# Kernel optimization log

Hardware: AMD Instinct MI355X
Metric: run time of the kernel (lower is better)

The kernel has to match this reference:

```python
import jax, jax.numpy as jnp
import numpy as np
from jax import lax

B, D, DEPTH, H, P, NP, IMG, PS = 16, 384, 6, 6, 2000, 4, 224, 16
N = (IMG // PS) ** 2  # 196 patches
T = N + 1             # +cls token
TEMP = 100.0
NEG = -100000.0


def layernorm(x, s, b, eps=1e-6):
    m = jnp.mean(x, -1, keepdims=True)
    v = jnp.var(x, -1, keepdims=True)
    return (x - m) * lax.rsqrt(v + eps) * s + b


def setup_inputs() -> dict:
    key = jax.random.key(0)
    ks = jax.random.split(key, 16)
    s = 0.02
    inp = {
        "x": jax.random.normal(ks[0], (B, 3, IMG, IMG), jnp.float32),
        "patch_w": jax.random.normal(ks[1], (D, 3, PS, PS), jnp.float32) * s,
        "patch_b": jnp.zeros((D,), jnp.float32),
        "cls_token": jax.random.normal(ks[2], (1, 1, D), jnp.float32) * s,
        "pos_embed": jax.random.normal(ks[3], (1, T, D), jnp.float32) * s,
        "ln1_s": jnp.ones((DEPTH, D), jnp.float32),
        "ln1_b": jnp.zeros((DEPTH, D), jnp.float32),
        "qkv_w": jax.random.normal(ks[4], (DEPTH, D, 3 * D), jnp.float32) * s,
        "qkv_b": jnp.zeros((DEPTH, 3 * D), jnp.float32),
        "proj_w": jax.random.normal(ks[5], (DEPTH, D, D), jnp.float32) * s,
        "proj_b": jnp.zeros((DEPTH, D), jnp.float32),
        "ln2_s": jnp.ones((DEPTH, D), jnp.float32),
        "ln2_b": jnp.zeros((DEPTH, D), jnp.float32),
        "fc1_w": jax.random.normal(ks[6], (DEPTH, D, 4 * D), jnp.float32) * s,
        "fc1_b": jnp.zeros((DEPTH, 4 * D), jnp.float32),
        "fc2_w": jax.random.normal(ks[7], (DEPTH, 4 * D, D), jnp.float32) * s,
        "fc2_b": jnp.zeros((DEPTH, D), jnp.float32),
        "norm_s": jnp.ones((D,), jnp.float32),
        "norm_b": jnp.zeros((D,), jnp.float32),
        "proto": jax.random.normal(ks[8], (P, D, NP), jnp.float32),
        "patch_select": jnp.full((1, P, NP), 0.1, jnp.float32),
    }
    return inp


def vit_features(x, patch_w, patch_b, cls_token, pos_embed, blk, norm_s, norm_b):
    # patch embed: non-overlapping 16x16 conv, NCHW/OIHW
    f = lax.conv_general_dilated(x, patch_w, (PS, PS), "VALID",
                                 dimension_numbers=("NCHW", "OIHW", "NCHW"))
    f = f + patch_b[None, :, None, None]              # (B, D, 14, 14)
    tok = f.reshape(B, D, N).transpose(0, 2, 1)        # (B, N, D)
    tok = jnp.concatenate([jnp.broadcast_to(cls_token, (B, 1, D)), tok], axis=1)
    tok = tok + pos_embed

    hd = D // H
    scale = hd ** -0.5

    def block(t, p):
        l1s, l1b, qw, qb, pw, pb, l2s, l2b, f1w, f1b, f2w, f2b = p
        h = layernorm(t, l1s, l1b)
        qkv = h @ qw + qb                              # (B, T, 3D)
        q, k, v = jnp.split(qkv, 3, axis=-1)
        q = q.reshape(B, T, H, hd).transpose(0, 2, 1, 3)
        k = k.reshape(B, T, H, hd).transpose(0, 2, 1, 3)
        v = v.reshape(B, T, H, hd).transpose(0, 2, 1, 3)
        att = jax.nn.softmax(jnp.einsum("bhqd,bhkd->bhqk", q, k) * scale, axis=-1)
        o = jnp.einsum("bhqk,bhkd->bhqd", att, v).transpose(0, 2, 1, 3).reshape(B, T, D)
        t = t + (o @ pw + pb)
        h = layernorm(t, l2s, l2b)
        t = t + (jax.nn.gelu(h @ f1w + f1b, approximate=False) @ f2w + f2b)
        return t, None

    tok, _ = lax.scan(block, tok, blk)
    tok = layernorm(tok, norm_s, norm_b)
    cls = tok[:, 0]                                    # (B, D)
    x_focal = tok[:, 1:] - cls[:, None, :]             # (B, N, D)
    feat = x_focal.transpose(0, 2, 1)                  # (B, D, N) == (B,D,14,14) flat
    return feat, cls


def reference(x, patch_w, patch_b, cls_token, pos_embed, ln1_s, ln1_b, qkv_w,
              qkv_b, proj_w, proj_b, ln2_s, ln2_b, fc1_w, fc1_b, fc2_w, fc2_b,
              norm_s, norm_b, proto, patch_select):
    blk = (ln1_s, ln1_b, qkv_w, qkv_b, proj_w, proj_b, ln2_s, ln2_b,
           fc1_w, fc1_b, fc2_w, fc2_b)
    feat, cls = vit_features(x, patch_w, patch_b, cls_token, pos_embed, blk,
                             norm_s, norm_b)
    # L2-normalize over channel dim (torch F.normalize, eps=1e-12)
    fn = feat / jnp.maximum(jnp.linalg.norm(feat, axis=1, keepdims=True), 1e-12)
    pn = proto / jnp.maximum(jnp.linalg.norm(proto, axis=1, keepdims=True), 1e-12)
    # cosine sims for every (prototype, patch, subpatch): (B, P, N, NP)
    dist = jnp.einsum("bdn,pdk->bpnk", fn, pn).reshape(B, P, N * NP)

    slots = jax.nn.sigmoid(patch_select * TEMP)        # (1, P, NP)
    factor = slots.sum(-1, keepdims=True) + 1e-10

    mask = jnp.ones((B, P, N * NP), dist.dtype)
    col = jnp.arange(N * NP)
    vals = []
    for _ in range(NP):  # greedy non-overlapping subpatch matching
        dm = dist + (1.0 - mask) * NEG
        ids = jnp.argmax(dm, axis=-1)                  # (B, P)
        vals.append(jnp.take_along_axis(dm, ids[..., None], axis=-1)[..., 0])
        mask = jnp.where(col[None, None, :] == ids[..., None], 0.0, mask)
    values = jnp.stack(vals, axis=-1)                  # (B, P, NP)
    proto_scores = (values * (slots * NP / factor)).sum(-1)  # (B, P)
    return cls, proto_scores
```

## Files before the change

kernel.cpp:

```cpp
#include <hip/hip_runtime.h>
#include <hip/hip_bf16.h>
#include <math.h>


#define MROWS 3152

typedef short bf16x8 __attribute__((ext_vector_type(8)));
typedef float f32x4 __attribute__((ext_vector_type(4)));
typedef unsigned short u16;

__device__ __forceinline__ void async_copy16(void* lds, const void* g) {
    __builtin_amdgcn_global_load_lds((const __attribute__((address_space(1))) unsigned int*)g,
                                     (__attribute__((address_space(3))) unsigned int*)lds,
                                     16, 0, 0);
}

__device__ __forceinline__ u16 f2b(float x) {
    __hip_bfloat16 h = __float2bfloat16(x);
    return *(u16*)&h;
}

__global__ void k_cvt(const float* __restrict__ in, __hip_bfloat16* __restrict__ o, int n) {
    int i = blockIdx.x * 256 + threadIdx.x;
    if (i < n) o[i] = __float2bfloat16(in[i]);
}

__global__ __launch_bounds__(256) void k_wt(const float* __restrict__ W, __hip_bfloat16* __restrict__ Wt,
                                            int K, int N) {
    __shared__ float t[32][33];
    const float* src = W + (size_t)blockIdx.z * K * N;
    __hip_bfloat16* dst = Wt + (size_t)blockIdx.z * K * N;
    int n0 = blockIdx.x * 32, k0 = blockIdx.y * 32;
    int tx = threadIdx.x & 31, ty = threadIdx.x >> 5;
    #pragma unroll
    for (int i = 0; i < 4; ++i) t[ty + i * 8][tx] = src[(size_t)(k0 + ty + i * 8) * N + n0 + tx];
    __syncthreads();
    #pragma unroll
    for (int i = 0; i < 4; ++i)
        dst[(size_t)(n0 + ty + i * 8) * K + k0 + tx] = __float2bfloat16(t[tx][ty + i * 8]);
}

__global__ void k_im2col(const float* __restrict__ x, __hip_bfloat16* __restrict__ Acol) {
    int idx = blockIdx.x * 256 + threadIdx.x;
    int k = idx % 768;
    int m = idx / 768;
    int b = m / 196, n = m % 196;
    int c = k >> 8, rem = k & 255, i = rem >> 4, j = rem & 15;
    int py = n / 14, px = n % 14;
    Acol[idx] = __float2bfloat16(x[((b * 3 + c) * 224 + py * 16 + i) * 224 + px * 16 + j]);
}

template<int RES, int GELU, int BF16OUT>
__global__ __launch_bounds__(256) void k_mfma_gemm(
    const u16* __restrict__ A, const u16* __restrict__ Bt,
    const float* __restrict__ bias, const float* __restrict__ res,
    float* __restrict__ Cf, __hip_bfloat16* __restrict__ Cb,
    int M, int N, int K)
{
    __shared__ u16 As[2][128 * 64];
    __shared__ u16 Bs[2][128 * 64];
    const int tid = threadIdx.x;
    const int wid = tid >> 6, lane = tid & 63;
    const int m0 = blockIdx.y * 128, n0 = blockIdx.x * 128;
    const int srow = tid >> 3;
    const int selem = (tid & 7) << 3;
    const int wm = (wid >> 1) * 64, wn = (wid & 1) * 64;

    f32x4 acc[4][4] = {};

    auto stage = [&](int buf, int kb) {
        #pragma unroll
        for (int g = 0; g < 4; ++g) {
            int r = g * 32 + srow;
            int sw = selem ^ ((r & 7) << 3);
            int gr = m0 + r; if (gr > M - 1) gr = M - 1;
            async_copy16(&As[buf][r * 64 + selem], A + (size_t)gr * K + kb + sw);
            async_copy16(&Bs[buf][r * 64 + selem], Bt + (size_t)(n0 + r) * K + kb + sw);
        }
    };

    const int nk = K >> 6;
    stage(0, 0);
    __syncthreads();
    for (int t = 0; t < nk; ++t) {
        const int cur = t & 1;
        if (t + 1 < nk) stage(cur ^ 1, (t + 1) << 6);
        #pragma unroll
        for (int ks = 0; ks < 64; ks += 32) {
            const int kk = ks + ((lane >> 4) << 3);
            bf16x8 af[4], bfr[4];
            #pragma unroll
            for (int i = 0; i < 4; ++i) {
                int r = wm + i * 16 + (lane & 15);
                af[i] = *(const bf16x8*)&As[cur][r * 64 + (kk ^ ((r & 7) << 3))];
            }
            #pragma unroll
            for (int j = 0; j < 4; ++j) {
                int r = wn + j * 16 + (lane & 15);
                bfr[j] = *(const bf16x8*)&Bs[cur][r * 64 + (kk ^ ((r & 7) << 3))];
            }
            #pragma unroll
            for (int i = 0; i < 4; ++i)
                #pragma unroll
                for (int j = 0; j < 4; ++j)
                    acc[i][j] = __builtin_amdgcn_mfma_f32_16x16x32_bf16(af[i], bfr[j], acc[i][j], 0, 0, 0);
        }
        __syncthreads();
    }
    const int cl = lane & 15, rg = (lane >> 4) << 2;
    #pragma unroll
    for (int i = 0; i < 4; ++i) {
        #pragma unroll
        for (int j = 0; j < 4; ++j) {
            const int col = n0 + wn + j * 16 + cl;
            const float bv = bias[col];
            #pragma unroll
            for (int r = 0; r < 4; ++r) {
                const int row = m0 + wm + i * 16 + rg + r;
                if (row >= M) continue;
                float v = acc[i][j][r] + bv;
                if (RES) v += res[(size_t)row * N + col];
                if (GELU) v = 0.5f * v * (1.0f + erff(v * 0.70710678118f));
                if (BF16OUT) Cb[(size_t)row * N + col] = __float2bfloat16(v);
                else         Cf[(size_t)row * N + col] = v;
            }
        }
    }
}

template<int RES, int GELU, int BF16OUT>
__global__ __launch_bounds__(256) void k_mfma_gemm64(
    const u16* __restrict__ A, const u16* __restrict__ Bt,
    const float* __restrict__ bias, const float* __restrict__ res,
    float* __restrict__ Cf, __hip_bfloat16* __restrict__ Cb,
    int M, int N, int K)
{
    __shared__ u16 As[2][128 * 64];
    __shared__ u16 Bs[2][64 * 64];
    const int tid = threadIdx.x;
    const int wid = tid >> 6, lane = tid & 63;
    const int m0 = blockIdx.y * 128, n0 = blockIdx.x * 64;
    const int srow = tid >> 3;
    const int selem = (tid & 7) << 3;
    const int wm = wid * 32;

    f32x4 acc[2][4] = {};

    auto stage = [&](int buf, int kb) {
        #pragma unroll
        for (int g = 0; g < 4; ++g) {
            int r = g * 32 + srow;
            int sw = selem ^ ((r & 7) << 3);
            int gr = m0 + r; if (gr > M - 1) gr = M - 1;
            async_copy16(&As[buf][r * 64 + selem], A + (size_t)gr * K + kb + sw);
        }
        #pragma unroll
        for (int g = 0; g < 2; ++g) {
            int r = g * 32 + srow;
            int sw = selem ^ ((r & 7) << 3);
            async_copy16(&Bs[buf][r * 64 + selem], Bt + (size_t)(n0 + r) * K + kb + sw);
        }
    };

    const int nk = K >> 6;
    stage(0, 0);
    __syncthreads();
    for (int t = 0; t < nk; ++t) {
        const int cur = t & 1;
        if (t + 1 < nk) stage(cur ^ 1, (t + 1) << 6);
        #pragma unroll
        for (int ks = 0; ks < 64; ks += 32) {
            const int kk = ks + ((lane >> 4) << 3);
            bf16x8 af[2], bfr[4];
            #pragma unroll
            for (int i = 0; i < 2; ++i) {
                int r = wm + i * 16 + (lane & 15);
                af[i] = *(const bf16x8*)&As[cur][r * 64 + (kk ^ ((r & 7) << 3))];
            }
            #pragma unroll
            for (int j = 0; j < 4; ++j) {
                int r = j * 16 + (lane & 15);
                bfr[j] = *(const bf16x8*)&Bs[cur][r * 64 + (kk ^ ((r & 7) << 3))];
            }
            #pragma unroll
            for (int i = 0; i < 2; ++i)
                #pragma unroll
                for (int j = 0; j < 4; ++j)
                    acc[i][j] = __builtin_amdgcn_mfma_f32_16x16x32_bf16(af[i], bfr[j], acc[i][j], 0, 0, 0);
        }
        __syncthreads();
    }
    const int cl = lane & 15, rg = (lane >> 4) << 2;
    #pragma unroll
    for (int i = 0; i < 2; ++i) {
        #pragma unroll
        for (int j = 0; j < 4; ++j) {
            const int col = n0 + j * 16 + cl;
            const float bv = bias[col];
            #pragma unroll
            for (int r = 0; r < 4; ++r) {
                const int row = m0 + wm + i * 16 + rg + r;
                if (row >= M) continue;
                float v = acc[i][j][r] + bv;
                if (RES) v += res[(size_t)row * N + col];
                if (GELU) v = 0.5f * v * (1.0f + erff(v * 0.70710678118f));
                if (BF16OUT) Cb[(size_t)row * N + col] = __float2bfloat16(v);
                else         Cf[(size_t)row * N + col] = v;
            }
        }
    }
}

__global__ void k_assemble(const float* __restrict__ ptmp, const float* __restrict__ cls_tok,
                           const float* __restrict__ pos, float* __restrict__ tok) {
    int idx = blockIdx.x * 256 + threadIdx.x;
    int d = idx % 384;
    int t = (idx / 384) % 197;
    int b = idx / (384 * 197);
    float v = (t == 0) ? cls_tok[d] : ptmp[((size_t)b * 196 + t - 1) * 384 + d];
    tok[idx] = v + pos[t * 384 + d];
}

template<typename OT>
__global__ __launch_bounds__(256) void k_ln(const float* __restrict__ X, const float* __restrict__ s,
                                            const float* __restrict__ bb, OT* __restrict__ Y, int rows) {
    int wid = threadIdx.x >> 6, lane = threadIdx.x & 63;
    int row = blockIdx.x * 4 + wid;
    if (row >= rows) return;
    const float* x = X + (size_t)row * 384;
    float v[6], sum = 0.f, sq = 0.f;
    #pragma unroll
    for (int i = 0; i < 6; ++i) { float t = x[lane + 64 * i]; v[i] = t; sum += t; sq += t * t; }
    #pragma unroll
    for (int m = 32; m > 0; m >>= 1) { sum += __shfl_xor(sum, m); sq += __shfl_xor(sq, m); }
    float mean = sum * (1.f / 384.f);
    float var  = sq * (1.f / 384.f) - mean * mean;
    float rstd = rsqrtf(var + 1e-6f);
    OT* y = Y + (size_t)row * 384;
    #pragma unroll
    for (int i = 0; i < 6; ++i) {
        int d = lane + 64 * i;
        float o = (v[i] - mean) * rstd * s[d] + bb[d];
        y[d] = (OT)o;
    }
}

__global__ __launch_bounds__(256) void k_attn_mfma(const u16* __restrict__ qkv, u16* __restrict__ o) {
    __shared__ u16 Ks[208 * 64];
    __shared__ u16 VT[64 * 256];
    __shared__ u16 Pl[4][16 * 256];
    const int bh = blockIdx.x;
    const int b = bh / 6, hh = bh % 6;
    const u16* base = qkv + (size_t)b * 197 * 1152 + hh * 64;
    const int tid = threadIdx.x, wid = tid >> 6, lane = tid & 63;

    for (int i = tid; i < 64 * 59; i += 256) {
        int d = i / 59, k = 197 + i % 59;
        VT[d * 256 + (k ^ ((d & 7) << 3))] = 0;
    }
    for (int i = tid; i < 64 * 48; i += 256) {
        int q = i / 48, k = 208 + i % 48;
        Pl[q >> 4][(q & 15) * 256 + (k ^ ((q & 7) << 3))] = 0;
    }
    for (int i = tid; i < 197 * 8; i += 256) {
        int r = i >> 3, cc = (i & 7) << 3;
        uint4 v = *(const uint4*)(base + (size_t)r * 1152 + 384 + cc);
        *(uint4*)&Ks[r * 64 + (cc ^ ((r & 7) << 3))] = v;
    }
    for (int i = tid; i < 197 * 8; i += 256) {
        int r = i >> 3, d0 = (i & 7) << 3;
        uint4 v = *(const uint4*)(base + (size_t)r * 1152 + 768 + d0);
        const u16* pv = (const u16*)&v;
        #pragma unroll
        for (int j = 0; j < 8; ++j) {
            int d = d0 + j;
            VT[d * 256 + (r ^ ((d & 7) << 3))] = pv[j];
        }
    }
    __syncthreads();

    const int g = lane >> 4, c = lane & 15;
    const int t0 = blockIdx.y * 7;
    const int nt = blockIdx.y ? 6 : 7;
    for (int t = wid; t < nt; t += 4) {
        const int qt = t0 + t;
        const int q0 = qt * 16;
        int qrow = q0 + c; if (qrow > 196) qrow = 196;
        bf16x8 aq[2];
        aq[0] = *(const bf16x8*)(base + (size_t)qrow * 1152 + g * 8);
        aq[1] = *(const bf16x8*)(base + (size_t)qrow * 1152 + 32 + g * 8);

        f32x4 acc[13] = {};
        #pragma unroll
        for (int j = 0; j < 13; ++j) {
            int kr = j * 16 + c;
            bf16x8 b0 = *(const bf16x8*)&Ks[kr * 64 + ((g * 8) ^ ((kr & 7) << 3))];
            bf16x8 b1 = *(const bf16x8*)&Ks[kr * 64 + ((32 + g * 8) ^ ((kr & 7) << 3))];
            acc[j] = __builtin_amdgcn_mfma_f32_16x16x32_bf16(aq[0], b0, acc[j], 0, 0, 0);
            acc[j] = __builtin_amdgcn_mfma_f32_16x16x32_bf16(aq[1], b1, acc[j], 0, 0, 0);
        }

        float sc[13][4];
        float mr[4] = {-1e30f, -1e30f, -1e30f, -1e30f};
        #pragma unroll
        for (int j = 0; j < 13; ++j) {
            bool valid = (j * 16 + c) < 197;
            #pragma unroll
            for (int r = 0; r < 4; ++r) {
                float v = valid ? acc[j][r] * 0.125f : -1e30f;
                sc[j][r] = v;
                mr[r] = fmaxf(mr[r], v);
            }
        }
        #pragma unroll
        for (int r = 0; r < 4; ++r) {
            #pragma unroll
            for (int msk = 1; msk <= 8; msk <<= 1) mr[r] = fmaxf(mr[r], __shfl_xor(mr[r], msk));
        }
        float lr[4] = {0.f, 0.f, 0.f, 0.f};
        #pragma unroll
        for (int j = 0; j < 13; ++j)
            #pragma unroll
            for (int r = 0; r < 4; ++r) { float e = __expf(sc[j][r] - mr[r]); sc[j][r] = e; lr[r] += e; }
        #pragma unroll
        for (int r = 0; r < 4; ++r) {
            #pragma unroll
            for (int msk = 1; msk <= 8; msk <<= 1) lr[r] += __shfl_xor(lr[r], msk);
            lr[r] = 1.f / lr[r];
        }
        #pragma unroll
        for (int j = 0; j < 13; ++j) {
            int col = j * 16 + c;
            #pragma unroll
            for (int r = 0; r < 4; ++r) {
                int q = g * 4 + r;
                Pl[wid][q * 256 + (col ^ ((q & 7) << 3))] = f2b(sc[j][r] * lr[r]);
            }
        }
        asm volatile("s_waitcnt lgkmcnt(0)" ::: "memory");

        f32x4 av[4] = {};
        #pragma unroll
        for (int ks = 0; ks < 7; ++ks) {
            int kk = ks * 32 + g * 8;
            bf16x8 ap = *(const bf16x8*)&Pl[wid][c * 256 + (kk ^ ((c & 7) << 3))];
            #pragma unroll
            for (int jd = 0; jd < 4; ++jd) {
                int dr = jd * 16 + c;
                bf16x8 bv = *(const bf16x8*)&VT[dr * 256 + (kk ^ ((dr & 7) << 3))];
                av[jd] = __builtin_amdgcn_mfma_f32_16x16x32_bf16(ap, bv, av[jd], 0, 0, 0);
            }
        }
        #pragma unroll
        for (int jd = 0; jd < 4; ++jd) {
            #pragma unroll
            for (int r = 0; r < 4; ++r) {
                int q = q0 + g * 4 + r;
                if (q < 197)
                    o[((size_t)b * 197 + q) * 384 + hh * 64 + jd * 16 + c] = f2b(av[jd][r]);
            }
        }
    }
}

__global__ __launch_bounds__(256) void k_fn(const float* __restrict__ tokn, __hip_bfloat16* __restrict__ fn,
                                            float* __restrict__ out) {
    int wid = threadIdx.x >> 6, lane = threadIdx.x & 63;
    int row = blockIdx.x * 4 + wid;
    int b = row / 196, n = row % 196;
    const float* xr = tokn + ((size_t)b * 197 + 1 + n) * 384;
    const float* cr = tokn + (size_t)b * 197 * 384;
    float v[6], ss = 0.f;
    #pragma unroll
    for (int i = 0; i < 6; ++i) {
        int d = lane + 64 * i;
        float t = xr[d] - cr[d];
        v[i] = t; ss += t * t;
    }
    #pragma unroll
    for (int m = 32; m > 0; m >>= 1) ss += __shfl_xor(ss, m);
    float inv = 1.f / fmaxf(sqrtf(ss), 1e-12f);
    #pragma unroll
    for (int i = 0; i < 6; ++i) fn[(size_t)row * 384 + lane + 64 * i] = __float2bfloat16(v[i] * inv);
    int idx = blockIdx.x * 256 + threadIdx.x;
    if (idx < 6144) out[idx] = tokn[(size_t)(idx / 384) * 197 * 384 + idx % 384];
}

__global__ __launch_bounds__(256) void k_pn(const float* __restrict__ proto, __hip_bfloat16* __restrict__ pn) {
    int p = blockIdx.x;
    int k = threadIdx.x >> 6, lane = threadIdx.x & 63;
    float v[6], ss = 0.f;
    #pragma unroll
    for (int i = 0; i < 6; ++i) {
        int d = lane + 64 * i;
        float t = proto[((size_t)p * 384 + d) * 4 + k];
        v[i] = t; ss += t * t;
    }
    #pragma unroll
    for (int m = 32; m > 0; m >>= 1) ss += __shfl_xor(ss, m);
    float inv = 1.f / fmaxf(sqrtf(ss), 1e-12f);
    #pragma unroll
    for (int i = 0; i < 6; ++i) pn[((size_t)p * 4 + k) * 384 + lane + 64 * i] = __float2bfloat16(v[i] * inv);
}

__device__ __forceinline__ void top4_insert(float v, float& t0, float& t1, float& t2, float& t3) {
    if (v > t3) {
        t3 = v;
        if (t3 > t2) { float t = t2; t2 = t3; t3 = t; }
        if (t2 > t1) { float t = t1; t1 = t2; t2 = t; }
        if (t1 > t0) { float t = t0; t0 = t1; t1 = t; }
    }
}

__global__ __launch_bounds__(256) void k_dist_mfma(
    const __hip_bfloat16* __restrict__ fnb, const __hip_bfloat16* __restrict__ pnb,
    const float* __restrict__ psel, float* __restrict__ out)
{
    __shared__ u16 Ap[128 * 64];
    __shared__ u16 Bf[208 * 64];
    const u16* fn = (const u16*)fnb;
    const u16* pn = (const u16*)pnb;
    const int b = blockIdx.x;
    const int pb = blockIdx.y;
    const int tid = threadIdx.x, wid = tid >> 6, lane = tid & 63;
    const int srow = tid >> 3;
    const int selem = (tid & 7) << 3;

    f32x4 acc[2][13] = {};

    for (int kt = 0; kt < 384; kt += 64) {
        __syncthreads();
        #pragma unroll
        for (int g = 0; g < 4; ++g) {
            int r = g * 32 + srow;
            int gr = pb * 128 + r; if (gr > 7999) gr = 7999;
            async_copy16(&Ap[r * 64 + selem],
                         pn + (size_t)gr * 384 + kt + (selem ^ ((r & 7) << 3)));
        }
        #pragma unroll
        for (int g = 0; g < 7; ++g) {
            int r = g * 32 + srow;
            if (r < 208) {
                int fr = r > 195 ? 195 : r;
                async_copy16(&Bf[r * 64 + selem],
                             fn + ((size_t)b * 196 + fr) * 384 + kt + (selem ^ ((r & 7) << 3)));
            }
        }
        __syncthreads();
        #pragma unroll
        for (int ks = 0; ks < 64; ks += 32) {
            const int kk = ks + ((lane >> 4) << 3);
            bf16x8 af[2];
            #pragma unroll
            for (int i = 0; i < 2; ++i) {
                int r = wid * 32 + i * 16 + (lane & 15);
                af[i] = *(const bf16x8*)&Ap[r * 64 + (kk ^ ((r & 7) << 3))];
            }
            #pragma unroll
            for (int j = 0; j < 13; ++j) {
                int r = j * 16 + (lane & 15);
                bf16x8 bj = *(const bf16x8*)&Bf[r * 64 + (kk ^ ((r & 7) << 3))];
                acc[0][j] = __builtin_amdgcn_mfma_f32_16x16x32_bf16(af[0], bj, acc[0][j], 0, 0, 0);
                acc[1][j] = __builtin_amdgcn_mfma_f32_16x16x32_bf16(af[1], bj, acc[1][j], 0, 0, 0);
            }
        }
    }
    const int cl = lane & 15;
    #pragma unroll
    for (int mi = 0; mi < 2; ++mi) {
        float t0 = -1e30f, t1 = -1e30f, t2 = -1e30f, t3 = -1e30f;
        #pragma unroll
        for (int j = 0; j < 13; ++j) {
            if (j * 16 + cl >= 196) continue;
            #pragma unroll
            for (int r = 0; r < 4; ++r) top4_insert(acc[mi][j][r], t0, t1, t2, t3);
        }
        #pragma unroll
        for (int m = 1; m <= 8; m <<= 1) {
            float u0 = __shfl_xor(t0, m), u1 = __shfl_xor(t1, m);
            float u2 = __shfl_xor(t2, m), u3 = __shfl_xor(t3, m);
            top4_insert(u0, t0, t1, t2, t3);
            top4_insert(u1, t0, t1, t2, t3);
            top4_insert(u2, t0, t1, t2, t3);
            top4_insert(u3, t0, t1, t2, t3);
        }
        if (cl == 0) {
            int proto = pb * 32 + wid * 8 + mi * 4 + (lane >> 4);
            if (proto < 2000) {
                float sl[4], fac = 1e-10f;
                #pragma unroll
                for (int i = 0; i < 4; ++i) {
                    sl[i] = 1.f / (1.f + expf(-psel[proto * 4 + i] * 100.f));
                    fac += sl[i];
                }
                float score = (t0 * sl[0] + t1 * sl[1] + t2 * sl[2] + t3 * sl[3]) * 4.f / fac;
                out[6144 + (size_t)b * 2000 + proto] = score;
            }
        }
    }
}

extern "C" void kernel_launch(void* const* d_in, const int* in_sizes, int n_in,
                              void* d_out, int out_size, void* d_ws, size_t ws_size,
                              hipStream_t stream) {
    const float* x       = (const float*)d_in[0];
    const float* patch_w = (const float*)d_in[1];
    const float* patch_b = (const float*)d_in[2];
    const float* cls_tok = (const float*)d_in[3];
    const float* pos     = (const float*)d_in[4];
    const float* ln1_s   = (const float*)d_in[5];
    const float* ln1_b   = (const float*)d_in[6];
    const float* qkv_w   = (const float*)d_in[7];
    const float* qkv_b   = (const float*)d_in[8];
    const float* proj_w  = (const float*)d_in[9];
    const float* proj_b  = (const float*)d_in[10];
    const float* ln2_s   = (const float*)d_in[11];
    const float* ln2_b   = (const float*)d_in[12];
    const float* fc1_w   = (const float*)d_in[13];
    const float* fc1_b   = (const float*)d_in[14];
    const float* fc2_w   = (const float*)d_in[15];
    const float* fc2_b   = (const float*)d_in[16];
    const float* norm_s  = (const float*)d_in[17];
    const float* norm_b  = (const float*)d_in[18];
    const float* proto   = (const float*)d_in[19];
    const float* psel    = (const float*)d_in[20];
    float* out = (float*)d_out;
    char* w = (char*)d_ws;

    __hip_bfloat16* wPb  = (__hip_bfloat16*)(w);
    __hip_bfloat16* wQ   = (__hip_bfloat16*)(w + 589824);
    __hip_bfloat16* wPr  = (__hip_bfloat16*)(w + 5898240);
    __hip_bfloat16* wF1  = (__hip_bfloat16*)(w + 7667712);
    __hip_bfloat16* wF2  = (__hip_bfloat16*)(w + 14745600);
    __hip_bfloat16* Acol = (__hip_bfloat16*)(w + 21823488);
    float*          ptmp = (float*)         (w + 26640384);
    float*          tok  = (float*)         (w + 31457280);
    __hip_bfloat16* hbf  = (__hip_bfloat16*)(w + 36298752);
    __hip_bfloat16* qkvb = (__hip_bfloat16*)(w + 38719488);
    __hip_bfloat16* aob  = (__hip_bfloat16*)(w + 53243904);
    __hip_bfloat16* hbig = (__hip_bfloat16*)(w + 55664640);
    float*          hf   = (float*)         (w + 65347584);
    __hip_bfloat16* fnb  = (__hip_bfloat16*)(w + 70189056);
    __hip_bfloat16* pnb  = (__hip_bfloat16*)(w + 72597504);

    k_cvt<<<1152, 256, 0, stream>>>(patch_w, wPb, 294912);
    k_wt<<<dim3(36, 12, 6), 256, 0, stream>>>(qkv_w, wQ, 384, 1152);
    k_wt<<<dim3(12, 12, 6), 256, 0, stream>>>(proj_w, wPr, 384, 384);
    k_wt<<<dim3(48, 12, 6), 256, 0, stream>>>(fc1_w, wF1, 384, 1536);
    k_wt<<<dim3(12, 48, 6), 256, 0, stream>>>(fc2_w, wF2, 1536, 384);

    k_im2col<<<9408, 256, 0, stream>>>(x, Acol);
    k_mfma_gemm64<0,0,0><<<dim3(6, 25), 256, 0, stream>>>(
        (const u16*)Acol, (const u16*)wPb, patch_b, nullptr, ptmp, nullptr, 3136, 384, 768);
    k_assemble<<<4728, 256, 0, stream>>>(ptmp, cls_tok, pos, tok);

    for (int l = 0; l < 6; ++l) {
        k_ln<__hip_bfloat16><<<788, 256, 0, stream>>>(tok, ln1_s + l * 384, ln1_b + l * 384, hbf, MROWS);
        k_mfma_gemm<0,0,1><<<dim3(9, 25), 256, 0, stream>>>(
            (const u16*)hbf, (const u16*)(wQ + (size_t)l * 1152 * 384), qkv_b + l * 1152,
            nullptr, nullptr, qkvb, MROWS, 1152, 384);
        k_attn_mfma<<<dim3(96, 2), 256, 0, stream>>>((const u16*)qkvb, (u16*)aob);
        k_mfma_gemm64<1,0,0><<<dim3(6, 25), 256, 0, stream>>>(
            (const u16*)aob, (const u16*)(wPr + (size_t)l * 384 * 384), proj_b + l * 384,
            tok, tok, nullptr, MROWS, 384, 384);
        k_ln<__hip_bfloat16><<<788, 256, 0, stream>>>(tok, ln2_s + l * 384, ln2_b + l * 384, hbf, MROWS);
        k_mfma_gemm<0,1,1><<<dim3(12, 25), 256, 0, stream>>>(
            (const u16*)hbf, (const u16*)(wF1 + (size_t)l * 1536 * 384), fc1_b + l * 1536,
            nullptr, nullptr, hbig, MROWS, 1536, 384);
        k_mfma_gemm64<1,0,0><<<dim3(6, 25), 256, 0, stream>>>(
            (const u16*)hbig, (const u16*)(wF2 + (size_t)l * 384 * 1536), fc2_b + l * 384,
            tok, tok, nullptr, MROWS, 384, 1536);
    }

    k_ln<float><<<788, 256, 0, stream>>>(tok, norm_s, norm_b, hf, MROWS);
    k_fn<<<784, 256, 0, stream>>>(hf, fnb, out);
    k_pn<<<2000, 256, 0, stream>>>(proto, pnb);
    k_dist_mfma<<<dim3(16, 63), 256, 0, stream>>>(fnb, pnb, psel, out);
}
```

Baseline: 685.6 us.

## Fuse layernorm into GEMM prologues and merge prep kernels into one launch

LayerNorm is folded into the QKV and FC1 GEMMs. Each block computes row statistics, then normalizes fp32 tokens into bf16 LDS tiles while staging B asynchronously, so the separate LN kernels and the hbf round-trip go away. All weight conversion, transposes, im2col, prototype normalization and cls-token init are merged into a single k_prep launch. Patch-embed now writes tokens plus pos embedding directly, and final LN is fused with feature normalization. This cuts launches and memory traffic, but the GEMM blocks take on redundant per-tile LN statistic work and register pressure.

```diff
diff --git a/kernel.cpp b/kernel.cpp
--- a/kernel.cpp
+++ b/kernel.cpp
@@ -20,18 +20,14 @@
     return *(u16*)&h;
 }
 
-__global__ void k_cvt(const float* __restrict__ in, __hip_bfloat16* __restrict__ o, int n) {
-    int i = blockIdx.x * 256 + threadIdx.x;
-    if (i < n) o[i] = __float2bfloat16(in[i]);
-}
-
-__global__ __launch_bounds__(256) void k_wt(const float* __restrict__ W, __hip_bfloat16* __restrict__ Wt,
-                                            int K, int N) {
-    __shared__ float t[32][33];
-    const float* src = W + (size_t)blockIdx.z * K * N;
-    __hip_bfloat16* dst = Wt + (size_t)blockIdx.z * K * N;
-    int n0 = blockIdx.x * 32, k0 = blockIdx.y * 32;
-    int tx = threadIdx.x & 31, ty = threadIdx.x >> 5;
+__device__ __forceinline__ void wt_tile(const float* __restrict__ W, __hip_bfloat16* __restrict__ Wt,
+                                        int K, int N, int id, int ntx, int perlayer,
+                                        float (*t)[33], int tid) {
+    int z = id / perlayer, rem = id % perlayer;
+    int n0 = (rem % ntx) * 32, k0 = (rem / ntx) * 32;
+    const float* src = W + (size_t)z * K * N;
+    __hip_bfloat16* dst = Wt + (size_t)z * K * N;
+    int tx = tid & 31, ty = tid >> 5;
     #pragma unroll
     for (int i = 0; i < 4; ++i) t[ty + i * 8][tx] = src[(size_t)(k0 + ty + i * 8) * N + n0 + tx];
     __syncthreads();
@@ -40,33 +36,82 @@
         dst[(size_t)(n0 + ty + i * 8) * K + k0 + tx] = __float2bfloat16(t[tx][ty + i * 8]);
 }
 
-__global__ void k_im2col(const float* __restrict__ x, __hip_bfloat16* __restrict__ Acol) {
-    int idx = blockIdx.x * 256 + threadIdx.x;
-    int k = idx % 768;
-    int m = idx / 768;
-    int b = m / 196, n = m % 196;
-    int c = k >> 8, rem = k & 255, i = rem >> 4, j = rem & 15;
-    int py = n / 14, px = n % 14;
-    Acol[idx] = __float2bfloat16(x[((b * 3 + c) * 224 + py * 16 + i) * 224 + px * 16 + j]);
-}
-
-template<int RES, int GELU, int BF16OUT>
-__global__ __launch_bounds__(256) void k_mfma_gemm(
+__global__ __launch_bounds__(256) void k_prep(
+    const float* __restrict__ patch_w, __hip_bfloat16* __restrict__ wPb,
+    const float* __restrict__ cls_tok, const float* __restrict__ pos, float* __restrict__ tok,
+    const float* __restrict__ qkv_w, __hip_bfloat16* __restrict__ wQ,
+    const float* __restrict__ proj_w, __hip_bfloat16* __restrict__ wPr,
+    const float* __restrict__ fc1_w, __hip_bfloat16* __restrict__ wF1,
+    const float* __restrict__ fc2_w, __hip_bfloat16* __restrict__ wF2,
+    const float* __restrict__ x, __hip_bfloat16* __restrict__ Acol,
+    const float* __restrict__ proto, __hip_bfloat16* __restrict__ pn)
+{
+    __shared__ float t[32][33];
+    int bid = blockIdx.x;
+    const int tid = threadIdx.x;
+    if (bid < 1152) {
+        int i = bid * 256 + tid;
+        wPb[i] = __float2bfloat16(patch_w[i]);
+        if (i < 6144) {
+            int b = i / 384, d = i % 384;
+            tok[(size_t)b * 197 * 384 + d] = cls_tok[d] + pos[d];
+        }
+        return;
+    }
+    bid -= 1152;
+    if (bid < 2592) { wt_tile(qkv_w, wQ, 384, 1152, bid, 36, 432, t, tid); return; }
+    bid -= 2592;
+    if (bid < 864)  { wt_tile(proj_w, wPr, 384, 384, bid, 12, 144, t, tid); return; }
+    bid -= 864;
+    if (bid < 3456) { wt_tile(fc1_w, wF1, 384, 1536, bid, 48, 576, t, tid); return; }
+    bid -= 3456;
+    if (bid < 3456) { wt_tile(fc2_w, wF2, 1536, 384, bid, 12, 576, t, tid); return; }
+    bid -= 3456;
+    if (bid < 9408) {
+        int idx = bid * 256 + tid;
+        int k = idx % 768, m = idx / 768;
+        int b = m / 196, n = m % 196;
+        int c = k >> 8, rem = k & 255, i = rem >> 4, j = rem & 15;
+        int py = n / 14, px = n % 14;
+        Acol[idx] = __float2bfloat16(x[((b * 3 + c) * 224 + py * 16 + i) * 224 + px * 16 + j]);
+        return;
+    }
+    bid -= 9408;
+    {
+        int p = bid;
+        int k = tid >> 6, lane = tid & 63;
+        float v[6], ss = 0.f;
+        #pragma unroll
+        for (int i = 0; i < 6; ++i) {
+            int d = lane + 64 * i;
+            float tv = proto[((size_t)p * 384 + d) * 4 + k];
+            v[i] = tv; ss += tv * tv;
+        }
+        #pragma unroll
+        for (int m = 32; m > 0; m >>= 1) ss += __shfl_xor(ss, m);
+        float inv = 1.f / fmaxf(sqrtf(ss), 1e-12f);
+        #pragma unroll
+        for (int i = 0; i < 6; ++i)
+            pn[((size_t)p * 4 + k) * 384 + lane + 64 * i] = __float2bfloat16(v[i] * inv);
+    }
+}
+
+__global__ __launch_bounds__(256) void k_patch_tok(
     const u16* __restrict__ A, const u16* __restrict__ Bt,
-    const float* __restrict__ bias, const float* __restrict__ res,
-    float* __restrict__ Cf, __hip_bfloat16* __restrict__ Cb,
-    int M, int N, int K)
+    const float* __restrict__ bias, const float* __restrict__ pos,
+    float* __restrict__ tok)
 {
+    const int M = 3136, K = 768;
     __shared__ u16 As[2][128 * 64];
-    __shared__ u16 Bs[2][128 * 64];
+    __shared__ u16 Bs[2][64 * 64];
     const int tid = threadIdx.x;
     const int wid = tid >> 6, lane = tid & 63;
-    const int m0 = blockIdx.y * 128, n0 = blockIdx.x * 128;
+    const int m0 = blockIdx.y * 128, n0 = blockIdx.x * 64;
     const int srow = tid >> 3;
     const int selem = (tid & 7) << 3;
-    const int wm = (wid >> 1) * 64, wn = (wid & 1) * 64;
-
-    f32x4 acc[4][4] = {};
+    const int wm = wid * 32;
+
+    f32x4 acc[2][4] = {};
 
     auto stage = [&](int buf, int kb) {
         #pragma unroll
@@ -75,6 +120,11 @@
             int sw = selem ^ ((r & 7) << 3);
             int gr = m0 + r; if (gr > M - 1) gr = M - 1;
             async_copy16(&As[buf][r * 64 + selem], A + (size_t)gr * K + kb + sw);
+        }
+        #pragma unroll
+        for (int g = 0; g < 2; ++g) {
+            int r = g * 32 + srow;
+            int sw = selem ^ ((r & 7) << 3);
             async_copy16(&Bs[buf][r * 64 + selem], Bt + (size_t)(n0 + r) * K + kb + sw);
         }
     };
@@ -88,6 +138,126 @@
         #pragma unroll
         for (int ks = 0; ks < 64; ks += 32) {
             const int kk = ks + ((lane >> 4) << 3);
+            bf16x8 af[2], bfr[4];
+            #pragma unroll
+            for (int i = 0; i < 2; ++i) {
+                int r = wm + i * 16 + (lane & 15);
+                af[i] = *(const bf16x8*)&As[cur][r * 64 + (kk ^ ((r & 7) << 3))];
+            }
+            #pragma unroll
+            for (int j = 0; j < 4; ++j) {
+                int r = j * 16 + (lane & 15);
+                bfr[j] = *(const bf16x8*)&Bs[cur][r * 64 + (kk ^ ((r & 7) << 3))];
+            }
+            #pragma unroll
+            for (int i = 0; i < 2; ++i)
+                #pragma unroll
+                for (int j = 0; j < 4; ++j)
+                    acc[i][j] = __builtin_amdgcn_mfma_f32_16x16x32_bf16(af[i], bfr[j], acc[i][j], 0, 0, 0);
+        }
+        __syncthreads();
+    }
+    const int cl = lane & 15, rg = (lane >> 4) << 2;
+    #pragma unroll
+    for (int i = 0; i < 2; ++i) {
+        #pragma unroll
+        for (int j = 0; j < 4; ++j) {
+            const int col = n0 + j * 16 + cl;
+            const float bv = bias[col];
+            #pragma unroll
+            for (int r = 0; r < 4; ++r) {
+                const int row = m0 + wm + i * 16 + rg + r;
+                if (row >= M) continue;
+                int b = row / 196, n = row % 196;
+                float v = acc[i][j][r] + bv + pos[(size_t)(1 + n) * 384 + col];
+                tok[((size_t)b * 197 + 1 + n) * 384 + col] = v;
+            }
+        }
+    }
+}
+
+template<int GELU>
+__global__ __launch_bounds__(256) void k_gemm_ln(
+    const float* __restrict__ tokf, const float* __restrict__ lns, const float* __restrict__ lnb,
+    const u16* __restrict__ Bt, const float* __restrict__ bias,
+    u16* __restrict__ Cb, int N)
+{
+    __shared__ u16 As[2][128 * 64];
+    __shared__ u16 Bs[2][128 * 64];
+    __shared__ float st[128][2];
+    __shared__ __align__(16) float sg[384];
+    __shared__ __align__(16) float bg[384];
+    const int tid = threadIdx.x, wid = tid >> 6, lane = tid & 63;
+    const int m0 = blockIdx.y * 128, n0 = blockIdx.x * 128;
+    const int srow = tid >> 3, selem = (tid & 7) << 3;
+    const int wm = (wid >> 1) * 64, wn = (wid & 1) * 64;
+
+    for (int i = tid; i < 384; i += 256) { sg[i] = lns[i]; bg[i] = lnb[i]; }
+    for (int i = 0; i < 32; ++i) {
+        int rl = wid + 4 * i;
+        int gr = m0 + rl; if (gr > MROWS - 1) gr = MROWS - 1;
+        const float* xr = tokf + (size_t)gr * 384;
+        float sum = 0.f, sq = 0.f;
+        #pragma unroll
+        for (int j = 0; j < 6; ++j) { float tv = xr[lane + 64 * j]; sum += tv; sq += tv * tv; }
+        #pragma unroll
+        for (int m = 32; m > 0; m >>= 1) { sum += __shfl_xor(sum, m); sq += __shfl_xor(sq, m); }
+        if (lane == 0) {
+            float mean = sum * (1.f / 384.f);
+            st[rl][0] = mean;
+            st[rl][1] = rsqrtf(sq * (1.f / 384.f) - mean * mean + 1e-6f);
+        }
+    }
+    __syncthreads();
+
+    const int r_ = tid >> 1, half = tid & 1, c0 = half * 32;
+    const float mean = st[r_][0], rstd = st[r_][1];
+    int gr_ = m0 + r_; if (gr_ > MROWS - 1) gr_ = MROWS - 1;
+    const float* arow = tokf + (size_t)gr_ * 384;
+
+    float4 areg[8];
+    auto loadA = [&](int kb) {
+        #pragma unroll
+        for (int c = 0; c < 8; ++c) areg[c] = *(const float4*)(arow + kb + c0 + c * 4);
+    };
+    auto writeA = [&](int buf, int kb) {
+        #pragma unroll
+        for (int c = 0; c < 4; ++c) {
+            const int colb = kb + c0 + c * 8;
+            float4 s0 = *(const float4*)&sg[colb], s1 = *(const float4*)&sg[colb + 4];
+            float4 b0 = *(const float4*)&bg[colb], b1 = *(const float4*)&bg[colb + 4];
+            float va[8] = {areg[2*c].x, areg[2*c].y, areg[2*c].z, areg[2*c].w,
+                           areg[2*c+1].x, areg[2*c+1].y, areg[2*c+1].z, areg[2*c+1].w};
+            float ss[8] = {s0.x, s0.y, s0.z, s0.w, s1.x, s1.y, s1.z, s1.w};
+            float bb[8] = {b0.x, b0.y, b0.z, b0.w, b1.x, b1.y, b1.z, b1.w};
+            bf16x8 pk;
+            #pragma unroll
+            for (int e = 0; e < 8; ++e)
+                pk[e] = (short)f2b((va[e] - mean) * rstd * ss[e] + bb[e]);
+            int chunk = (half * 4 + c) ^ (r_ & 7);
+            *(bf16x8*)&As[buf][r_ * 64 + chunk * 8] = pk;
+        }
+    };
+    auto stageB = [&](int buf, int kb) {
+        #pragma unroll
+        for (int g = 0; g < 4; ++g) {
+            int r = g * 32 + srow;
+            int sw = selem ^ ((r & 7) << 3);
+            async_copy16(&Bs[buf][r * 64 + selem], Bt + (size_t)(n0 + r) * 384 + kb + sw);
+        }
+    };
+
+    f32x4 acc[4][4] = {};
+    loadA(0);
+    stageB(0, 0);
+    writeA(0, 0);
+    __syncthreads();
+    for (int t = 0; t < 6; ++t) {
+        const int cur = t & 1;
+        if (t < 5) { loadA((t + 1) << 6); stageB(cur ^ 1, (t + 1) << 6); }
+        #pragma unroll
+        for (int ks = 0; ks < 64; ks += 32) {
+            const int kk = ks + ((lane >> 4) << 3);
             bf16x8 af[4], bfr[4];
             #pragma unroll
             for (int i = 0; i < 4; ++i) {
@@ -105,6 +275,7 @@
                 for (int j = 0; j < 4; ++j)
                     acc[i][j] = __builtin_amdgcn_mfma_f32_16x16x32_bf16(af[i], bfr[j], acc[i][j], 0, 0, 0);
         }
+        if (t < 5) writeA(cur ^ 1, (t + 1) << 6);
         __syncthreads();
     }
     const int cl = lane & 15, rg = (lane >> 4) << 2;
@@ -117,12 +288,10 @@
             #pragma unroll
             for (int r = 0; r < 4; ++r) {
                 const int row = m0 + wm + i * 16 + rg + r;
-                if (row >= M) continue;
+                if (row >= MROWS) continue;
                 float v = acc[i][j][r] + bv;
-                if (RES) v += res[(size_t)row * N + col];
                 if (GELU) v = 0.5f * v * (1.0f + erff(v * 0.70710678118f));
-                if (BF16OUT) Cb[(size_t)row * N + col] = __float2bfloat16(v);
-                else         Cf[(size_t)row * N + col] = v;
+                Cb[(size_t)row * N + col] = f2b(v);
             }
         }
     }
@@ -211,40 +380,6 @@
     }
 }
 
-__global__ void k_assemble(const float* __restrict__ ptmp, const float* __restrict__ cls_tok,
-                           const float* __restrict__ pos, float* __restrict__ tok) {
-    int idx = blockIdx.x * 256 + threadIdx.x;
-    int d = idx % 384;
-    int t = (idx / 384) % 197;
-    int b = idx / (384 * 197);
-    float v = (t == 0) ? cls_tok[d] : ptmp[((size_t)b * 196 + t - 1) * 384 + d];
-    tok[idx] = v + pos[t * 384 + d];
-}
-
-template<typename OT>
-__global__ __launch_bounds__(256) void k_ln(const float* __restrict__ X, const float* __restrict__ s,
-                                            const float* __restrict__ bb, OT* __restrict__ Y, int rows) {
-    int wid = threadIdx.x >> 6, lane = threadIdx.x & 63;
-    int row = blockIdx.x * 4 + wid;
-    if (row >= rows) return;
-    const float* x = X + (size_t)row * 384;
-    float v[6], sum = 0.f, sq = 0.f;
-    #pragma unroll
-    for (int i = 0; i < 6; ++i) { float t = x[lane + 64 * i]; v[i] = t; sum += t; sq += t * t; }
-    #pragma unroll
-    for (int m = 32; m > 0; m >>= 1) { sum += __shfl_xor(sum, m); sq += __shfl_xor(sq, m); }
-    float mean = sum * (1.f / 384.f);
-    float var  = sq * (1.f / 384.f) - mean * mean;
-    float rstd = rsqrtf(var + 1e-6f);
-    OT* y = Y + (size_t)row * 384;
-    #pragma unroll
-    for (int i = 0; i < 6; ++i) {
-        int d = lane + 64 * i;
-        float o = (v[i] - mean) * rstd * s[d] + bb[d];
-        y[d] = (OT)o;
-    }
-}
-
 __global__ __launch_bounds__(256) void k_attn_mfma(const u16* __restrict__ qkv, u16* __restrict__ o) {
     __shared__ u16 Ks[208 * 64];
     __shared__ u16 VT[64 * 256];
@@ -283,8 +418,7 @@
     const int t0 = blockIdx.y * 7;
     const int nt = blockIdx.y ? 6 : 7;
     for (int t = wid; t < nt; t += 4) {
-        const int qt = t0 + t;
-        const int q0 = qt * 16;
+        const int q0 = (t0 + t) * 16;
         int qrow = q0 + c; if (qrow > 196) qrow = 196;
         bf16x8 aq[2];
         aq[0] = *(const bf16x8*)(base + (size_t)qrow * 1152 + g * 8);
@@ -363,44 +497,47 @@
     }
 }
 
-__global__ __launch_bounds__(256) void k_fn(const float* __restrict__ tokn, __hip_bfloat16* __restrict__ fn,
-                                            float* __restrict__ out) {
+__device__ __forceinline__ void lnvals(const float* __restrict__ x, const float* __restrict__ s,
+                                       const float* __restrict__ bb, int lane, float* v) {
+    float sum = 0.f, sq = 0.f;
+    #pragma unroll
+    for (int i = 0; i < 6; ++i) { float t = x[lane + 64 * i]; v[i] = t; sum += t; sq += t * t; }
+    #pragma unroll
+    for (int m = 32; m > 0; m >>= 1) { sum += __shfl_xor(sum, m); sq += __shfl_xor(sq, m); }
+    float mean = sum * (1.f / 384.f);
+    float var  = sq * (1.f / 384.f) - mean * mean;
+    float rstd = rsqrtf(var + 1e-6f);
+    #pragma unroll
+    for (int i = 0; i < 6; ++i) {
+        int d = lane + 64 * i;
+        v[i] = (v[i] - mean) * rstd * s[d] + bb[d];
+    }
+}
+
+__global__ __launch_bounds__(256) void k_fnln(const float* __restrict__ tok, const float* __restrict__ s,
+                                              const float* __restrict__ bb, u16* __restrict__ fnb,
+                                              float* __restrict__ out) {
     int wid = threadIdx.x >> 6, lane = threadIdx.x & 63;
     int row = blockIdx.x * 4 + wid;
-    int b = row / 196, n = row % 196;
-    const float* xr = tokn + ((size_t)b * 197 + 1 + n) * 384;
-    const float* cr = tokn + (size_t)b * 197 * 384;
-    float v[6], ss = 0.f;
-    #pragma unroll
-    for (int i = 0; i < 6; ++i) {
-        int d = lane + 64 * i;
-        float t = xr[d] - cr[d];
-        v[i] = t; ss += t * t;
-    }
-    #pragma unroll
-    for (int m = 32; m > 0; m >>= 1) ss += __shfl_xor(ss, m);
-    float inv = 1.f / fmaxf(sqrtf(ss), 1e-12f);
-    #pragma unroll
-    for (int i = 0; i < 6; ++i) fn[(size_t)row * 384 + lane + 64 * i] = __float2bfloat16(v[i] * inv);
-    int idx = blockIdx.x * 256 + threadIdx.x;
-    if (idx < 6144) out[idx] = tokn[(size_t)(idx / 384) * 197 * 384 + idx % 384];
-}
-
-__global__ __launch_bounds__(256) void k_pn(const float* __restrict__ proto, __hip_bfloat16* __restrict__ pn) {
-    int p = blockIdx.x;
-    int k = threadIdx.x >> 6, lane = threadIdx.x & 63;
-    float v[6], ss = 0.f;
-    #pragma unroll
-    for (int i = 0; i < 6; ++i) {
-        int d = lane + 64 * i;
-        float t = proto[((size_t)p * 384 + d) * 4 + k];
-        v[i] = t; ss += t * t;
-    }
-    #pragma unroll
-    for (int m = 32; m > 0; m >>= 1) ss += __shfl_xor(ss, m);
-    float inv = 1.f / fmaxf(sqrtf(ss), 1e-12f);
-    #pragma unroll
-    for (int i = 0; i < 6; ++i) pn[((size_t)p * 4 + k) * 384 + lane + 64 * i] = __float2bfloat16(v[i] * inv);
+    int b = row / 197, t = row % 197;
+    float v1[6];
+    lnvals(tok + (size_t)row * 384, s, bb, lane, v1);
+    if (t == 0) {
+        #pragma unroll
+        for (int i = 0; i < 6; ++i) out[(size_t)b * 384 + lane + 64 * i] = v1[i];
+    } else {
+        float v0[6];
+        lnvals(tok + (size_t)b * 197 * 384, s, bb, lane, v0);
+        float d[6], ss = 0.f;
+        #pragma unroll
+        for (int i = 0; i < 6; ++i) { d[i] = v1[i] - v0[i]; ss += d[i] * d[i]; }
+        #pragma unroll
+        for (int m = 32; m > 0; m >>= 1) ss += __shfl_xor(ss, m);
+        float inv = 1.f / fmaxf(sqrtf(ss), 1e-12f);
+        #pragma unroll
+        for (int i = 0; i < 6; ++i)
+            fnb[((size_t)b * 196 + t - 1) * 384 + lane + 64 * i] = f2b(d[i] * inv);
+    }
 }
 
 __device__ __forceinline__ void top4_insert(float v, float& t0, float& t1, float& t2, float& t3) {
@@ -528,52 +665,42 @@
     char* w = (char*)d_ws;
 
     __hip_bfloat16* wPb  = (__hip_bfloat16*)(w);
-    __hip_bfloat16* wQ   = (__hip_bfloat16*)(w + 589824);
-    __hip_bfloat16* wPr  = (__hip_bfloat16*)(w + 5898240);
-    __hip_bfloat16* wF1  = (__hip_bfloat16*)(w + 7667712);
-    __hip_bfloat16* wF2  = (__hip_bfloat16*)(w + 14745600);
+    u16*            wQ   = (u16*)(w + 589824);
+    u16*            wPr  = (u16*)(w + 5898240);
+    u16*            wF1  = (u16*)(w + 7667712);
+    u16*            wF2  = (u16*)(w + 14745600);
     __hip_bfloat16* Acol = (__hip_bfloat16*)(w + 21823488);
-    float*          ptmp = (float*)         (w + 26640384);
     float*          tok  = (float*)         (w + 31457280);
-    __hip_bfloat16* hbf  = (__hip_bfloat16*)(w + 36298752);
-    __hip_bfloat16* qkvb = (__hip_bfloat16*)(w + 38719488);
-    __hip_bfloat16* aob  = (__hip_bfloat16*)(w + 53243904);
-    __hip_bfloat16* hbig = (__hip_bfloat16*)(w + 55664640);
-    float*          hf   = (float*)         (w + 65347584);
-    __hip_bfloat16* fnb  = (__hip_bfloat16*)(w + 70189056);
+    u16*            qkvb = (u16*)(w + 38719488);
+    u16*            aob  = (u16*)(w + 53243904);
+    u16*            hbig = (u16*)(w + 55664640);
+    u16*            fnb  = (u16*)(w + 70189056);
     __hip_bfloat16* pnb  = (__hip_bfloat16*)(w + 72597504);
 
-    k_cvt<<<1152, 256, 0, stream>>>(patch_w, wPb, 294912);
-    k_wt<<<dim3(36, 12, 6), 256, 0, stream>>>(qkv_w, wQ, 384, 1152);
-    k_wt<<<dim3(12, 12, 6), 256, 0, stream>>>(proj_w, wPr, 384, 384);
-    k_wt<<<dim3(48, 12, 6), 256, 0, stream>>>(fc1_w, wF1, 384, 1536);
-    k_wt<<<dim3(12, 48, 6), 256, 0, stream>>>(fc2_w, wF2, 1536, 384);
-
-    k_im2col<<<9408, 256, 0, stream>>>(x, Acol);
-    k_mfma_gemm64<0,0,0><<<dim3(6, 25), 256, 0, stream>>>(
-        (const u16*)Acol, (const u16*)wPb, patch_b, nullptr, ptmp, nullptr, 3136, 384, 768);
-    k_assemble<<<4728, 256, 0, stream>>>(ptmp, cls_tok, pos, tok);
+    k_prep<<<22928, 256, 0, stream>>>(patch_w, wPb, cls_tok, pos, tok,
+                                      qkv_w, (__hip_bfloat16*)wQ,
+                                      proj_w, (__hip_bfloat16*)wPr,
+                                      fc1_w, (__hip_bfloat16*)wF1,
+                                      fc2_w, (__hip_bfloat16*)wF2,
+                                      x, Acol, proto, pnb);
+    k_patch_tok<<<dim3(6, 25), 256, 0, stream>>>((const u16*)Acol, (const u16*)wPb, patch_b, pos, tok);
 
     for (int l = 0; l < 6; ++l) {
-        k_ln<__hip_bfloat16><<<788, 256, 0, stream>>>(tok, ln1_s + l * 384, ln1_b + l * 384, hbf, MROWS);
-        k_mfma_gemm<0,0,1><<<dim3(9, 25), 256, 0, stream>>>(
-            (const u16*)hbf, (const u16*)(wQ + (size_t)l * 1152 * 384), qkv_b + l * 1152,
-            nullptr, nullptr, qkvb, MROWS, 1152, 384);
-        k_attn_mfma<<<dim3(96, 2), 256, 0, stream>>>((const u16*)qkvb, (u16*)aob);
+        k_gemm_ln<0><<<dim3(9, 25), 256, 0, stream>>>(
+            tok, ln1_s + l * 384, ln1_b + l * 384,
+            wQ + (size_t)l * 1152 * 384, qkv_b + l * 1152, qkvb, 1152);
+        k_attn_mfma<<<dim3(96, 2), 256, 0, stream>>>(qkvb, aob);
         k_mfma_gemm64<1,0,0><<<dim3(6, 25), 256, 0, stream>>>(
-            (const u16*)aob, (const u16*)(wPr + (size_t)l * 384 * 384), proj_b + l * 384,
+            aob, wPr + (size_t)l * 384 * 384, proj_b + l * 384,
             tok, tok, nullptr, MROWS, 384, 384);
-        k_ln<__hip_bfloat16><<<788, 256, 0, stream>>>(tok, ln2_s + l * 384, ln2_b + l * 384, hbf, MROWS);
-        k_mfma_gemm<0,1,1><<<dim3(12, 25), 256, 0, stream>>>(
-            (const u16*)hbf, (const u16*)(wF1 + (size_t)l * 1536 * 384), fc1_b + l * 1536,
-            nullptr, nullptr, hbig, MROWS, 1536, 384);
+        k_gemm_ln<1><<<dim3(12, 25), 256, 0, stream>>>(
+            tok, ln2_s + l * 384, ln2_b + l * 384,
+            wF1 + (size_t)l * 384 * 1536, fc1_b + l * 1536, hbig, 1536);
         k_mfma_gemm64<1,0,0><<<dim3(6, 25), 256, 0, stream>>>(
-            (const u16*)hbig, (const u16*)(wF2 + (size_t)l * 384 * 1536), fc2_b + l * 384,
+            hbig, wF2 + (size_t)l * 1536 * 384, fc2_b + l * 384,
             tok, tok, nullptr, MROWS, 384, 1536);
     }
 
-    k_ln<float><<<788, 256, 0, stream>>>(tok, norm_s, norm_b, hf, MROWS);
-    k_fn<<<784, 256, 0, stream>>>(hf, fnb, out);
-    k_pn<<<2000, 256, 0, stream>>>(proto, pnb);
-    k_dist_mfma<<<dim3(16, 63), 256, 0, stream>>>(fnb, pnb, psel, out);
-}
+    k_fnln<<<788, 256, 0, stream>>>(tok, norm_s, norm_b, fnb, out);
+    k_dist_mfma<<<dim3(16, 63), 256, 0, stream>>>((const __hip_bfloat16*)fnb, pnb, psel, out);
+}
```

Result: slower. 1.138 ms (+66.0%).
